# Kernel optimization log

Measured on AMD Instinct MI355X. Metric: run time of the kernel, lower is better.

Reference implementation:

```python
import jax, jax.numpy as jnp
import numpy as np

L1, L2, ALPHA, BETA, EPS = 0.5, 1.5, 1.0, 50000000.0, 1e-08


def tube(att, label):
    # per-row cosine/sine TUBE distance, fully vectorized over batch
    dot = jnp.sum(att * label, axis=-1)            # [B]
    p_norm = jnp.sqrt(jnp.sum(att * att, axis=-1))
    g_norm = jnp.sqrt(jnp.sum(label * label, axis=-1))
    denom = p_norm * g_norm
    cosine = jnp.where(denom == 0, 0.0, dot / jnp.where(denom == 0, 1.0, denom))
    s_s = 1.0 - jnp.square(cosine)
    # s_s < 0 -> sine = 0 ; s_s == 0 -> sqrt(s_s + eps) ; else sqrt(s_s)
    sine = jnp.where(s_s < 0, 0.0, jnp.sqrt(jnp.where(s_s <= 0, EPS, s_s)))
    r_all = p_norm * cosine / jnp.where(g_norm == 0, g_norm + EPS, g_norm)
    base = p_norm * sine + jnp.abs(g_norm - p_norm * cosine)
    ds = jnp.where(r_all >= 1, L1 * base,
         jnp.where(r_all >= 0, base,
                   L2 * jnp.abs(p_norm * cosine - g_norm - p_norm * sine)))
    ds = -jnp.log(jnp.tanh(1.0 / ds))
    return jnp.mean(ds)


def kl_loss(mu, logvar):
    return -0.5 * BETA * jnp.mean(1.0 + logvar - jnp.square(mu) - jnp.exp(logvar))


def cross_entropy(logits, label_idx):
    logp = jax.nn.log_softmax(logits, axis=-1)
    return -jnp.mean(jnp.take_along_axis(logp, label_idx[:, None], axis=1)[:, 0])


def setup_inputs() -> dict:
    key = jax.random.key(0)
    ks = jax.random.split(key, 12)
    B, C, D, Z = 16384, 100, 512, 128
    return {
        "fusion_out": jax.random.normal(ks[0], (B, C), jnp.float32),
        "comple_out": jax.random.normal(ks[1], (B, D), jnp.float32),
        "labels": jax.random.normal(ks[2], (B, C), jnp.float32),
        "labels_encoder": jax.random.normal(ks[3], (B, D), jnp.float32),
        "x_A": jax.random.normal(ks[4], (B, D), jnp.float32),
        "x_A_reconstructed": jax.random.normal(ks[5], (B, D), jnp.float32),
        "x_B": jax.random.normal(ks[6], (B, D), jnp.float32),
        "x_B_reconstructed": jax.random.normal(ks[7], (B, D), jnp.float32),
        "x_C": jax.random.normal(ks[8], (B, D), jnp.float32),
        "x_C_reconstructed": jax.random.normal(ks[9], (B, D), jnp.float32),
        "mu": jax.random.normal(ks[10], (B, Z), jnp.float32),
        "logvar": jax.random.normal(ks[11], (B, Z), jnp.float32),
    }


def reference(fusion_out, comple_out, labels, labels_encoder, x_A,
              x_A_reconstructed, x_B, x_B_reconstructed, x_C,
              x_C_reconstructed, mu, logvar):
    label_idx = jnp.argmax(labels, axis=1)
    tube_A = ALPHA * tube(x_A_reconstructed, x_A)
    tube_B = ALPHA * tube(x_B_reconstructed, x_B)
    tube_C = ALPHA * tube(x_C_reconstructed, x_C)
    kl = kl_loss(mu, logvar)
    st_all = ALPHA * tube(comple_out, labels_encoder)
    ce = cross_entropy(fusion_out, label_idx)
    return tube_A + tube_B + tube_C + kl + ce + st_all
```

## Files before the change

### kernel.cpp

```cpp
#include <hip/hip_runtime.h>
#include <math.h>

static constexpr float kL1   = 0.5f;
static constexpr float kL2   = 1.5f;
static constexpr float kBeta = 50000000.0f;
static constexpr float kEps  = 1e-08f;

__device__ __forceinline__ float waveSum(float v) {
#pragma unroll
    for (int off = 32; off > 0; off >>= 1) v += __shfl_xor(v, off, 64);
    return v;
}

__global__ __launch_bounds__(256) void fused_loss_kernel(
    const float* __restrict__ fusion_out, const float* __restrict__ comple_out,
    const float* __restrict__ labels,     const float* __restrict__ labels_enc,
    const float* __restrict__ xA,  const float* __restrict__ xAr,
    const float* __restrict__ xB,  const float* __restrict__ xBr,
    const float* __restrict__ xC,  const float* __restrict__ xCr,
    const float* __restrict__ mu,  const float* __restrict__ logvar,
    float* __restrict__ out,
    int B, int C, int D, int Z,
    int tubeBlocks, int klBlocks, int ceBlocks)
{
    const int lane = threadIdx.x & 63;
    const int wave = threadIdx.x >> 6;
    const int wavesPerBlock = blockDim.x >> 6;
    const int bid = blockIdx.x;

    float my = 0.0f;

    if (bid < tubeBlocks) {
        const int globalWave = bid * wavesPerBlock + wave;
        const int totalWaves = tubeBlocks * wavesPerBlock;
        const int totalRows  = 4 * B;
        const int d4 = D >> 2;
        float acc = 0.0f;
        for (int row = globalWave; row < totalRows; row += totalWaves) {
            const int pair = row / B;
            const int r    = row - pair * B;
            const float* att; const float* lab;
            if      (pair == 0) { att = xAr;        lab = xA;         }
            else if (pair == 1) { att = xBr;        lab = xB;         }
            else if (pair == 2) { att = xCr;        lab = xC;         }
            else                { att = comple_out; lab = labels_enc; }
            const float4* a4 = (const float4*)(att + (size_t)r * D);
            const float4* l4 = (const float4*)(lab + (size_t)r * D);
            float dot = 0.f, pp = 0.f, gg = 0.f;
            for (int c = lane; c < d4; c += 64) {
                float4 a = a4[c];
                float4 l = l4[c];
                dot += a.x * l.x + a.y * l.y + a.z * l.z + a.w * l.w;
                pp  += a.x * a.x + a.y * a.y + a.z * a.z + a.w * a.w;
                gg  += l.x * l.x + l.y * l.y + l.z * l.z + l.w * l.w;
            }
            dot = waveSum(dot);
            pp  = waveSum(pp);
            gg  = waveSum(gg);
            if (lane == 0) {
                float p_norm = sqrtf(pp);
                float g_norm = sqrtf(gg);
                float denom  = p_norm * g_norm;
                float cosine = (denom == 0.0f) ? 0.0f : dot / denom;
                float s_s    = 1.0f - cosine * cosine;
                float sine   = (s_s < 0.0f) ? 0.0f
                             : sqrtf((s_s <= 0.0f) ? kEps : s_s);
                float gd     = (g_norm == 0.0f) ? (g_norm + kEps) : g_norm;
                float pc     = p_norm * cosine;
                float r_all  = pc / gd;
                float base   = p_norm * sine + fabsf(g_norm - pc);
                float ds     = (r_all >= 1.0f) ? (kL1 * base)
                             : ((r_all >= 0.0f) ? base
                                                : kL2 * fabsf(pc - g_norm - p_norm * sine));
                acc += -logf(tanhf(1.0f / ds));
            }
        }
        my = acc / (float)B;
    } else if (bid < tubeBlocks + klBlocks) {
        const int b2 = bid - tubeBlocks;
        const int n4 = (B * Z) >> 2;
        const float4* mu4 = (const float4*)mu;
        const float4* lv4 = (const float4*)logvar;
        const int tid    = b2 * blockDim.x + threadIdx.x;
        const int stride = klBlocks * blockDim.x;
        float acc = 0.0f;
        for (int i = tid; i < n4; i += stride) {
            float4 m = mu4[i];
            float4 l = lv4[i];
            acc += (1.0f + l.x - m.x * m.x - __expf(l.x));
            acc += (1.0f + l.y - m.y * m.y - __expf(l.y));
            acc += (1.0f + l.z - m.z * m.z - __expf(l.z));
            acc += (1.0f + l.w - m.w * m.w - __expf(l.w));
        }
        my = acc * (-0.5f * kBeta / (float)(B * Z));
    } else {
        const int b3 = bid - tubeBlocks - klBlocks;
        const int globalWave = b3 * wavesPerBlock + wave;
        const int totalWaves = ceBlocks * wavesPerBlock;
        float acc = 0.0f;
        for (int r = globalWave; r < B; r += totalWaves) {
            const float* lrow = labels     + (size_t)r * C;
            const float* frow = fusion_out + (size_t)r * C;
            const bool has0 = (lane < C);
            const bool has1 = (lane + 64 < C);
            float v0 = has0 ? lrow[lane]      : -INFINITY;
            float v1 = has1 ? lrow[lane + 64] : -INFINITY;
            float f0 = has0 ? frow[lane]      : -INFINITY;
            float f1 = has1 ? frow[lane + 64] : -INFINITY;
            float bv; int bi;
            if (v1 > v0) { bv = v1; bi = lane + 64; } else { bv = v0; bi = lane; }
#pragma unroll
            for (int off = 32; off > 0; off >>= 1) {
                float ov = __shfl_xor(bv, off, 64);
                int   oi = __shfl_xor(bi, off, 64);
                if (ov > bv || (ov == bv && oi < bi)) { bv = ov; bi = oi; }
            }
            float m = fmaxf(f0, f1);
#pragma unroll
            for (int off = 32; off > 0; off >>= 1) m = fmaxf(m, __shfl_xor(m, off, 64));
            float e = 0.0f;
            if (has0) e += __expf(f0 - m);
            if (has1) e += __expf(f1 - m);
            e = waveSum(e);
            float t = (bi < 64) ? __shfl(f0, bi, 64) : __shfl(f1, bi - 64, 64);
            if (lane == 0) acc += -(t - m - __logf(e));
        }
        my = acc / (float)B;
    }

    float s = waveSum(my);
    __shared__ float sw[8];
    if (lane == 0) sw[wave] = s;
    __syncthreads();
    if (threadIdx.x == 0) {
        float tot = 0.0f;
        for (int i = 0; i < wavesPerBlock; ++i) tot += sw[i];
        atomicAdd(out, tot);
    }
}

extern "C" void kernel_launch(void* const* d_in, const int* in_sizes, int n_in,
                              void* d_out, int out_size, void* d_ws, size_t ws_size,
                              hipStream_t stream) {
    const float* fusion_out = (const float*)d_in[0];
    const float* comple_out = (const float*)d_in[1];
    const float* labels     = (const float*)d_in[2];
    const float* labels_enc = (const float*)d_in[3];
    const float* xA  = (const float*)d_in[4];
    const float* xAr = (const float*)d_in[5];
    const float* xB  = (const float*)d_in[6];
    const float* xBr = (const float*)d_in[7];
    const float* xC  = (const float*)d_in[8];
    const float* xCr = (const float*)d_in[9];
    const float* mu  = (const float*)d_in[10];
    const float* lv  = (const float*)d_in[11];
    float* out = (float*)d_out;

    const int B = 16384;
    const int C = in_sizes[0] / B;
    const int D = in_sizes[1] / B;
    const int Z = in_sizes[10] / B;

    const int tubeBlocks = 4096;
    const int klBlocks   = 512;
    const int ceBlocks   = 512;
    const int totalBlocks = tubeBlocks + klBlocks + ceBlocks;

    hipMemsetAsync(out, 0, sizeof(float), stream);
    fused_loss_kernel<<<totalBlocks, 256, 0, stream>>>(
        fusion_out, comple_out, labels, labels_enc,
        xA, xAr, xB, xBr, xC, xCr, mu, lv,
        out, B, C, D, Z, tubeBlocks, klBlocks, ceBlocks);
}
```

Measured before the change: 299.9 us.

## Process one tube row per 16-lane group and use fast tanh-log math

The tube reduction now gives each row to a 16-lane group instead of a whole wave. Each group does 8 unrolled float4 loads per input, so a wave has four rows in flight, and the cross-lane reductions are shorter. The -log(tanh(1/ds)) term is rewritten with __expf/__logf as log(1+e^-2t) - log(1-e^-2t), with a clamp near zero. The CE block count also goes up. The fixed unroll bound of 8 assumes D<=512, and the fast-math form changes precision.

```diff
diff --git a/kernel.cpp b/kernel.cpp
--- a/kernel.cpp
+++ b/kernel.cpp
@@ -9,6 +9,12 @@
 __device__ __forceinline__ float waveSum(float v) {
 #pragma unroll
     for (int off = 32; off > 0; off >>= 1) v += __shfl_xor(v, off, 64);
+    return v;
+}
+
+__device__ __forceinline__ float groupSum16(float v) {
+#pragma unroll
+    for (int off = 8; off > 0; off >>= 1) v += __shfl_xor(v, off, 64);
     return v;
 }
 
@@ -31,12 +37,14 @@
     float my = 0.0f;
 
     if (bid < tubeBlocks) {
-        const int globalWave = bid * wavesPerBlock + wave;
-        const int totalWaves = tubeBlocks * wavesPerBlock;
-        const int totalRows  = 4 * B;
-        const int d4 = D >> 2;
+        const int sub   = lane & 15;
+        const int grp   = lane >> 4;
+        const int globalGroup = (bid * wavesPerBlock + wave) * 4 + grp;
+        const int totalGroups = tubeBlocks * wavesPerBlock * 4;
+        const int totalRows   = 4 * B;
+        const int k16 = D >> 6;
         float acc = 0.0f;
-        for (int row = globalWave; row < totalRows; row += totalWaves) {
+        for (int row = globalGroup; row < totalRows; row += totalGroups) {
             const int pair = row / B;
             const int r    = row - pair * B;
             const float* att; const float* lab;
@@ -47,17 +55,20 @@
             const float4* a4 = (const float4*)(att + (size_t)r * D);
             const float4* l4 = (const float4*)(lab + (size_t)r * D);
             float dot = 0.f, pp = 0.f, gg = 0.f;
-            for (int c = lane; c < d4; c += 64) {
-                float4 a = a4[c];
-                float4 l = l4[c];
-                dot += a.x * l.x + a.y * l.y + a.z * l.z + a.w * l.w;
-                pp  += a.x * a.x + a.y * a.y + a.z * a.z + a.w * a.w;
-                gg  += l.x * l.x + l.y * l.y + l.z * l.z + l.w * l.w;
+#pragma unroll
+            for (int k = 0; k < 8; ++k) {
+                if (k < k16) {
+                    float4 a = a4[sub + 16 * k];
+                    float4 l = l4[sub + 16 * k];
+                    dot += a.x * l.x + a.y * l.y + a.z * l.z + a.w * l.w;
+                    pp  += a.x * a.x + a.y * a.y + a.z * a.z + a.w * a.w;
+                    gg  += l.x * l.x + l.y * l.y + l.z * l.z + l.w * l.w;
+                }
             }
-            dot = waveSum(dot);
-            pp  = waveSum(pp);
-            gg  = waveSum(gg);
-            if (lane == 0) {
+            dot = groupSum16(dot);
+            pp  = groupSum16(pp);
+            gg  = groupSum16(gg);
+            if (sub == 0) {
                 float p_norm = sqrtf(pp);
                 float g_norm = sqrtf(gg);
                 float denom  = p_norm * g_norm;
@@ -72,7 +83,9 @@
                 float ds     = (r_all >= 1.0f) ? (kL1 * base)
                              : ((r_all >= 0.0f) ? base
                                                 : kL2 * fabsf(pc - g_norm - p_norm * sine));
-                acc += -logf(tanhf(1.0f / ds));
+                float t  = 1.0f / ds;
+                float em = __expf(-2.0f * t);
+                acc += __logf(1.0f + em) - __logf(fmaxf(1.0f - em, 1e-30f));
             }
         }
         my = acc / (float)B;
@@ -163,7 +176,7 @@
 
     const int tubeBlocks = 4096;
     const int klBlocks   = 512;
-    const int ceBlocks   = 512;
+    const int ceBlocks   = 2048;
     const int totalBlocks = tubeBlocks + klBlocks + ceBlocks;
 
     hipMemsetAsync(out, 0, sizeof(float), stream);
```

Measured after the change: 313.3 us. 4.4% more time.

## Split fused loss into separate kernels with 16-rows-per-wave tube reduction

Applied to the files above, without the earlier changes.

Replaces the single branchy fused kernel with separate tube, KL and CE kernels plus a final partial-sum reduction, dropping the memset and global atomics. The tube kernel now maps 16 rows per wave with 4 lanes per row, so most of the reduction needs only two shuffle steps and all lanes do the tail math. It also swaps -log(tanh(x)) for an exp/log formula using fast intrinsics. The cost is extra kernel launches, serialization of the three loss parts instead of running them concurrently, and a slightly different numerical path for the tanh term.

```diff
diff --git a/kernel.cpp b/kernel.cpp
--- a/kernel.cpp
+++ b/kernel.cpp
@@ -12,131 +12,162 @@
     return v;
 }
 
-__global__ __launch_bounds__(256) void fused_loss_kernel(
-    const float* __restrict__ fusion_out, const float* __restrict__ comple_out,
-    const float* __restrict__ labels,     const float* __restrict__ labels_enc,
+__device__ __forceinline__ float tubeTail(float dot, float pp, float gg) {
+    float p_norm = sqrtf(pp);
+    float g_norm = sqrtf(gg);
+    float denom  = p_norm * g_norm;
+    float cosine = (denom == 0.0f) ? 0.0f : dot / denom;
+    float s_s    = 1.0f - cosine * cosine;
+    float sine   = (s_s < 0.0f) ? 0.0f : sqrtf((s_s <= 0.0f) ? kEps : s_s);
+    float gd     = (g_norm == 0.0f) ? (g_norm + kEps) : g_norm;
+    float pc     = p_norm * cosine;
+    float r_all  = pc / gd;
+    float base   = p_norm * sine + fabsf(g_norm - pc);
+    float ds     = (r_all >= 1.0f) ? (kL1 * base)
+                 : ((r_all >= 0.0f) ? base
+                                    : kL2 * fabsf(pc - g_norm - p_norm * sine));
+    float t  = 1.0f / ds;
+    float em = __expf(-2.0f * t);
+    return __logf(1.0f + em) - __logf(fmaxf(1.0f - em, 1e-30f));
+}
+
+__global__ __launch_bounds__(256) void tube_kernel(
+    const float* __restrict__ comple_out, const float* __restrict__ labels_enc,
     const float* __restrict__ xA,  const float* __restrict__ xAr,
     const float* __restrict__ xB,  const float* __restrict__ xBr,
     const float* __restrict__ xC,  const float* __restrict__ xCr,
-    const float* __restrict__ mu,  const float* __restrict__ logvar,
-    float* __restrict__ out,
-    int B, int C, int D, int Z,
-    int tubeBlocks, int klBlocks, int ceBlocks)
+    float* __restrict__ partials)
 {
     const int lane = threadIdx.x & 63;
     const int wave = threadIdx.x >> 6;
-    const int wavesPerBlock = blockDim.x >> 6;
-    const int bid = blockIdx.x;
-
+    const int sub  = lane & 3;
+    const int grp  = lane >> 2;
+    const int B = 16384, D = 512;
+
+    const int gw      = blockIdx.x * 4 + wave;
+    const int rowBase = gw * 16;
+    const int pair    = rowBase >> 14;
+    const int r0      = rowBase & (B - 1);
+
+    const float* att; const float* lab;
+    if      (pair == 0) { att = xAr;        lab = xA;         }
+    else if (pair == 1) { att = xBr;        lab = xB;         }
+    else if (pair == 2) { att = xCr;        lab = xC;         }
+    else                { att = comple_out; lab = labels_enc; }
+
+    const float4* a4 = (const float4*)(att + (size_t)(r0 + grp) * D);
+    const float4* l4 = (const float4*)(lab + (size_t)(r0 + grp) * D);
+
+    float dot = 0.f, pp = 0.f, gg = 0.f;
+#pragma unroll 4
+    for (int k = 0; k < 32; ++k) {
+        float4 a = a4[sub + 4 * k];
+        float4 l = l4[sub + 4 * k];
+        dot += a.x * l.x + a.y * l.y + a.z * l.z + a.w * l.w;
+        pp  += a.x * a.x + a.y * a.y + a.z * a.z + a.w * a.w;
+        gg  += l.x * l.x + l.y * l.y + l.z * l.z + l.w * l.w;
+    }
+#pragma unroll
+    for (int off = 1; off <= 2; off <<= 1) {
+        dot += __shfl_xor(dot, off, 64);
+        pp  += __shfl_xor(pp,  off, 64);
+        gg  += __shfl_xor(gg,  off, 64);
+    }
     float my = 0.0f;
-
-    if (bid < tubeBlocks) {
-        const int globalWave = bid * wavesPerBlock + wave;
-        const int totalWaves = tubeBlocks * wavesPerBlock;
-        const int totalRows  = 4 * B;
-        const int d4 = D >> 2;
-        float acc = 0.0f;
-        for (int row = globalWave; row < totalRows; row += totalWaves) {
-            const int pair = row / B;
-            const int r    = row - pair * B;
-            const float* att; const float* lab;
-            if      (pair == 0) { att = xAr;        lab = xA;         }
-            else if (pair == 1) { att = xBr;        lab = xB;         }
-            else if (pair == 2) { att = xCr;        lab = xC;         }
-            else                { att = comple_out; lab = labels_enc; }
-            const float4* a4 = (const float4*)(att + (size_t)r * D);
-            const float4* l4 = (const float4*)(lab + (size_t)r * D);
-            float dot = 0.f, pp = 0.f, gg = 0.f;
-            for (int c = lane; c < d4; c += 64) {
-                float4 a = a4[c];
-                float4 l = l4[c];
-                dot += a.x * l.x + a.y * l.y + a.z * l.z + a.w * l.w;
-                pp  += a.x * a.x + a.y * a.y + a.z * a.z + a.w * a.w;
-                gg  += l.x * l.x + l.y * l.y + l.z * l.z + l.w * l.w;
-            }
-            dot = waveSum(dot);
-            pp  = waveSum(pp);
-            gg  = waveSum(gg);
-            if (lane == 0) {
-                float p_norm = sqrtf(pp);
-                float g_norm = sqrtf(gg);
-                float denom  = p_norm * g_norm;
-                float cosine = (denom == 0.0f) ? 0.0f : dot / denom;
-                float s_s    = 1.0f - cosine * cosine;
-                float sine   = (s_s < 0.0f) ? 0.0f
-                             : sqrtf((s_s <= 0.0f) ? kEps : s_s);
-                float gd     = (g_norm == 0.0f) ? (g_norm + kEps) : g_norm;
-                float pc     = p_norm * cosine;
-                float r_all  = pc / gd;
-                float base   = p_norm * sine + fabsf(g_norm - pc);
-                float ds     = (r_all >= 1.0f) ? (kL1 * base)
-                             : ((r_all >= 0.0f) ? base
-                                                : kL2 * fabsf(pc - g_norm - p_norm * sine));
-                acc += -logf(tanhf(1.0f / ds));
-            }
+    if (sub == 0) my = tubeTail(dot, pp, gg) / (float)B;
+
+    float s = waveSum(my);
+    __shared__ float sw[4];
+    if (lane == 0) sw[wave] = s;
+    __syncthreads();
+    if (threadIdx.x == 0)
+        partials[blockIdx.x] = sw[0] + sw[1] + sw[2] + sw[3];
+}
+
+__global__ __launch_bounds__(256) void kl_kernel(
+    const float* __restrict__ mu, const float* __restrict__ logvar,
+    float* __restrict__ partials, int n4)
+{
+    const int tid    = blockIdx.x * blockDim.x + threadIdx.x;
+    const int stride = gridDim.x * blockDim.x;
+    const float4* mu4 = (const float4*)mu;
+    const float4* lv4 = (const float4*)logvar;
+    float acc = 0.0f;
+    for (int i = tid; i < n4; i += stride) {
+        float4 m = mu4[i];
+        float4 l = lv4[i];
+        acc += (1.0f + l.x - m.x * m.x - __expf(l.x));
+        acc += (1.0f + l.y - m.y * m.y - __expf(l.y));
+        acc += (1.0f + l.z - m.z * m.z - __expf(l.z));
+        acc += (1.0f + l.w - m.w * m.w - __expf(l.w));
+    }
+    float my = acc * (-0.5f * kBeta / (float)(16384 * 128));
+    float s = waveSum(my);
+    __shared__ float sw[4];
+    const int lane = threadIdx.x & 63, wave = threadIdx.x >> 6;
+    if (lane == 0) sw[wave] = s;
+    __syncthreads();
+    if (threadIdx.x == 0)
+        partials[blockIdx.x] = sw[0] + sw[1] + sw[2] + sw[3];
+}
+
+__global__ __launch_bounds__(256) void ce_kernel(
+    const float* __restrict__ fusion_out, const float* __restrict__ labels,
+    float* __restrict__ partials, int B, int C)
+{
+    const int lane = threadIdx.x & 63;
+    const int wave = threadIdx.x >> 6;
+    const int globalWave = blockIdx.x * 4 + wave;
+    const int totalWaves = gridDim.x * 4;
+    float acc = 0.0f;
+    for (int r = globalWave; r < B; r += totalWaves) {
+        const float* lrow = labels     + (size_t)r * C;
+        const float* frow = fusion_out + (size_t)r * C;
+        const bool has0 = (lane < C);
+        const bool has1 = (lane + 64 < C);
+        float v0 = has0 ? lrow[lane]      : -INFINITY;
+        float v1 = has1 ? lrow[lane + 64] : -INFINITY;
+        float f0 = has0 ? frow[lane]      : -INFINITY;
+        float f1 = has1 ? frow[lane + 64] : -INFINITY;
+        float bv; int bi;
+        if (v1 > v0) { bv = v1; bi = lane + 64; } else { bv = v0; bi = lane; }
+#pragma unroll
+        for (int off = 32; off > 0; off >>= 1) {
+            float ov = __shfl_xor(bv, off, 64);
+            int   oi = __shfl_xor(bi, off, 64);
+            if (ov > bv || (ov == bv && oi < bi)) { bv = ov; bi = oi; }
         }
-        my = acc / (float)B;
-    } else if (bid < tubeBlocks + klBlocks) {
-        const int b2 = bid - tubeBlocks;
-        const int n4 = (B * Z) >> 2;
-        const float4* mu4 = (const float4*)mu;
-        const float4* lv4 = (const float4*)logvar;
-        const int tid    = b2 * blockDim.x + threadIdx.x;
-        const int stride = klBlocks * blockDim.x;
-        float acc = 0.0f;
-        for (int i = tid; i < n4; i += stride) {
-            float4 m = mu4[i];
-            float4 l = lv4[i];
-            acc += (1.0f + l.x - m.x * m.x - __expf(l.x));
-            acc += (1.0f + l.y - m.y * m.y - __expf(l.y));
-            acc += (1.0f + l.z - m.z * m.z - __expf(l.z));
-            acc += (1.0f + l.w - m.w * m.w - __expf(l.w));
-        }
-        my = acc * (-0.5f * kBeta / (float)(B * Z));
-    } else {
-        const int b3 = bid - tubeBlocks - klBlocks;
-        const int globalWave = b3 * wavesPerBlock + wave;
-        const int totalWaves = ceBlocks * wavesPerBlock;
-        float acc = 0.0f;
-        for (int r = globalWave; r < B; r += totalWaves) {
-            const float* lrow = labels     + (size_t)r * C;
-            const float* frow = fusion_out + (size_t)r * C;
-            const bool has0 = (lane < C);
-            const bool has1 = (lane + 64 < C);
-            float v0 = has0 ? lrow[lane]      : -INFINITY;
-            float v1 = has1 ? lrow[lane + 64] : -INFINITY;
-            float f0 = has0 ? frow[lane]      : -INFINITY;
-            float f1 = has1 ? frow[lane + 64] : -INFINITY;
-            float bv; int bi;
-            if (v1 > v0) { bv = v1; bi = lane + 64; } else { bv = v0; bi = lane; }
-#pragma unroll
-            for (int off = 32; off > 0; off >>= 1) {
-                float ov = __shfl_xor(bv, off, 64);
-                int   oi = __shfl_xor(bi, off, 64);
-                if (ov > bv || (ov == bv && oi < bi)) { bv = ov; bi = oi; }
-            }
-            float m = fmaxf(f0, f1);
-#pragma unroll
-            for (int off = 32; off > 0; off >>= 1) m = fmaxf(m, __shfl_xor(m, off, 64));
-            float e = 0.0f;
-            if (has0) e += __expf(f0 - m);
-            if (has1) e += __expf(f1 - m);
-            e = waveSum(e);
-            float t = (bi < 64) ? __shfl(f0, bi, 64) : __shfl(f1, bi - 64, 64);
-            if (lane == 0) acc += -(t - m - __logf(e));
-        }
-        my = acc / (float)B;
-    }
-
+        float m = fmaxf(f0, f1);
+#pragma unroll
+        for (int off = 32; off > 0; off >>= 1) m = fmaxf(m, __shfl_xor(m, off, 64));
+        float e = 0.0f;
+        if (has0) e += __expf(f0 - m);
+        if (has1) e += __expf(f1 - m);
+        e = waveSum(e);
+        float t = (bi < 64) ? __shfl(f0, bi, 64) : __shfl(f1, bi - 64, 64);
+        if (lane == 0) acc += -(t - m - __logf(e));
+    }
+    float my = acc / (float)B;
     float s = waveSum(my);
-    __shared__ float sw[8];
-    if (lane == 0) sw[wave] = s;
-    __syncthreads();
-    if (threadIdx.x == 0) {
-        float tot = 0.0f;
-        for (int i = 0; i < wavesPerBlock; ++i) tot += sw[i];
-        atomicAdd(out, tot);
-    }
+    __shared__ float sw[4];
+    if (lane == 0) sw[wave] = s;
+    __syncthreads();
+    if (threadIdx.x == 0)
+        partials[blockIdx.x] = sw[0] + sw[1] + sw[2] + sw[3];
+}
+
+__global__ __launch_bounds__(256) void reduce_partials(
+    const float* __restrict__ partials, float* __restrict__ out, int n)
+{
+    float s = 0.0f;
+    for (int i = threadIdx.x; i < n; i += 256) s += partials[i];
+    s = waveSum(s);
+    __shared__ float sw[4];
+    const int lane = threadIdx.x & 63;
+    const int wave = threadIdx.x >> 6;
+    if (lane == 0) sw[wave] = s;
+    __syncthreads();
+    if (threadIdx.x == 0) out[0] = sw[0] + sw[1] + sw[2] + sw[3];
 }
 
 extern "C" void kernel_launch(void* const* d_in, const int* in_sizes, int n_in,
@@ -155,20 +186,24 @@
     const float* mu  = (const float*)d_in[10];
     const float* lv  = (const float*)d_in[11];
     float* out = (float*)d_out;
+    float* ws  = (float*)d_ws;
 
     const int B = 16384;
     const int C = in_sizes[0] / B;
-    const int D = in_sizes[1] / B;
     const int Z = in_sizes[10] / B;
 
-    const int tubeBlocks = 4096;
-    const int klBlocks   = 512;
-    const int ceBlocks   = 512;
-    const int totalBlocks = tubeBlocks + klBlocks + ceBlocks;
-
-    hipMemsetAsync(out, 0, sizeof(float), stream);
-    fused_loss_kernel<<<totalBlocks, 256, 0, stream>>>(
-        fusion_out, comple_out, labels, labels_enc,
-        xA, xAr, xB, xBr, xC, xCr, mu, lv,
-        out, B, C, D, Z, tubeBlocks, klBlocks, ceBlocks);
-}
+    const int tubeBlocks = 1024;
+    const int klBlocks   = 256;
+    const int ceBlocks   = 2048;
+    const int totalP = tubeBlocks + klBlocks + ceBlocks;
+
+    float* pTube = ws;
+    float* pKl   = ws + tubeBlocks;
+    float* pCe   = ws + tubeBlocks + klBlocks;
+
+    tube_kernel<<<tubeBlocks, 256, 0, stream>>>(
+        comple_out, labels_enc, xA, xAr, xB, xBr, xC, xCr, pTube);
+    kl_kernel<<<klBlocks, 256, 0, stream>>>(mu, lv, pKl, (B * Z) / 4);
+    ce_kernel<<<ceBlocks, 256, 0, stream>>>(fusion_out, labels, pCe, B, C);
+    reduce_partials<<<1, 256, 0, stream>>>(ws, out, totalP);
+}
```

After: 294.1 us. Within noise of the previous version (-1.9%).
